# Performance work log

Measured on AMD Instinct MI355X. Metric: run time of the kernel, lower is better.

Reference implementation:

```python
import jax, jax.numpy as jnp
import numpy as np

D = 768       # input embedding dim
H = 256       # hidden_dim
NH = 4        # num_heads
HD = H // NH  # head_dim = 64
M = 131072    # number of candidate LLM embeddings


def setup_inputs() -> dict:
    key = jax.random.key(0)
    ks = jax.random.split(key, 16)
    s = 0.02
    return {
        "user": jax.random.normal(ks[0], (D,), jnp.float32),
        "query": jax.random.normal(ks[1], (D,), jnp.float32),
        "llm": jax.random.normal(ks[2], (M, D), jnp.float32),
        # projection weights (torch Linear: y = x @ W.T + b)
        "Wu": jax.random.normal(ks[3], (H, D), jnp.float32) * s,
        "bu": jnp.zeros((H,), jnp.float32),
        "Wq": jax.random.normal(ks[4], (H, D), jnp.float32) * s,
        "bq": jnp.zeros((H,), jnp.float32),
        "Wl": jax.random.normal(ks[5], (H, D), jnp.float32) * s,
        "bl": jnp.zeros((H,), jnp.float32),
        # MultiheadAttention packed in-projection [3H, H] and bias [3H]
        "in_proj_w": jax.random.normal(ks[6], (3 * H, H), jnp.float32) * s,
        "in_proj_b": jnp.zeros((3 * H,), jnp.float32),
        "out_proj_w": jax.random.normal(ks[7], (H, H), jnp.float32) * s,
        "out_proj_b": jnp.zeros((H,), jnp.float32),
        # final scoring linear: [1, 2H]
        "Wo": jax.random.normal(ks[8], (1, 2 * H), jnp.float32) * s,
        "bo": jnp.zeros((1,), jnp.float32),
    }


def reference(user, query, llm, Wu, bu, Wq, bq, Wl, bl,
              in_proj_w, in_proj_b, out_proj_w, out_proj_b, Wo, bo):
    m = llm.shape[0]
    # input projections
    u = user @ Wu.T + bu            # [H]
    qv = query @ Wq.T + bq          # [H]
    l = llm @ Wl.T + bl             # [M, H]
    # context rows are identical for every candidate -> compute K/V once on [2, H]
    ctx = jnp.stack([u, qv], axis=0)                      # [2, H]
    Wq_a, Wk_a, Wv_a = jnp.split(in_proj_w, 3, axis=0)    # each [H, H]
    bq_a, bk_a, bv_a = jnp.split(in_proj_b, 3, axis=0)
    q = (l @ Wq_a.T + bq_a).reshape(m, NH, HD)            # [M, nh, hd] (seq_len=1)
    k = (ctx @ Wk_a.T + bk_a).reshape(2, NH, HD)          # [2, nh, hd]
    v = (ctx @ Wv_a.T + bv_a).reshape(2, NH, HD)
    scale = 1.0 / jnp.sqrt(jnp.asarray(HD, q.dtype))
    scores = jnp.einsum('mhd,khd->mhk', q, k) * scale     # [M, nh, 2]
    attn = jax.nn.softmax(scores, axis=-1)
    attended = jnp.einsum('mhk,khd->mhd', attn, v).reshape(m, H)
    attended = attended @ out_proj_w.T + out_proj_b       # [M, H]
    x = jnp.concatenate([attended, l], axis=-1)           # [M, 2H]
    # out = Sequential(ReLU, Dropout(eval=identity), Linear(2H, 1))
    logits = (jax.nn.relu(x) @ Wo.T + bo).squeeze(-1)     # [M]
    return logits
```

## Files before the change

kernel.cpp:

```cpp
#include <hip/hip_runtime.h>


typedef float f32x4 __attribute__((ext_vector_type(4)));
typedef __bf16 bf16x8 __attribute__((ext_vector_type(8)));

__device__ __forceinline__ unsigned f2bf(float f) {
  unsigned u = __builtin_bit_cast(unsigned, f);
  u += 0x7fffu + ((u >> 16) & 1u);
  return u >> 16;
}

__device__ __forceinline__ void gl_lds16(const void* g, void* l) {
  __builtin_amdgcn_global_load_lds(
      (const __attribute__((address_space(1))) void*)g,
      (__attribute__((address_space(3))) void*)l, 16, 0, 0);
}

__global__ void prep_a(const float* __restrict__ user, const float* __restrict__ query,
                       const float* __restrict__ Wu, const float* __restrict__ bu,
                       const float* __restrict__ Wq, const float* __restrict__ bq,
                       float* __restrict__ wf) {
  const int og = threadIdx.x >> 5, ln = threadIdx.x & 31;
  const int o = blockIdx.x * 8 + og;
  const int isq = o >> 8, j = o & 255;
  const float* Wrow = (isq ? Wq : Wu) + (size_t)j * 768;
  const float* vec = isq ? query : user;
  float p = 0.f;
  #pragma unroll
  for (int i = 0; i < 24; ++i) { int d = ln * 24 + i; p = fmaf(Wrow[d], vec[d], p); }
  #pragma unroll
  for (int off = 16; off; off >>= 1) p += __shfl_xor(p, off);
  if (ln == 0) wf[o] = p + (isq ? bq[j] : bu[j]);
}

__global__ void prep_b(const float* __restrict__ ipw, const float* __restrict__ ipb,
                       float* __restrict__ wf) {
  const int og = threadIdx.x >> 5, ln = threadIdx.x & 31;
  const int o = blockIdx.x * 8 + og;
  const int kv = o >> 9, cc = (o >> 8) & 1, j = o & 255;
  const int row = 256 + kv * 256 + j;
  const float* Wrow = ipw + (size_t)row * 256;
  const float* ctx = wf + cc * 256;
  float p = 0.f;
  #pragma unroll
  for (int i = 0; i < 8; ++i) { int d = ln * 8 + i; p = fmaf(Wrow[d], ctx[d], p); }
  #pragma unroll
  for (int off = 16; off; off >>= 1) p += __shfl_xor(p, off);
  if (ln == 0) wf[512 + o] = p + ipb[row];
}

__global__ void prep_c(const float* __restrict__ ipw, const float* __restrict__ ipb,
                       const float* __restrict__ opw, const float* __restrict__ opb,
                       float* __restrict__ wf) {
  const int t = threadIdx.x, b = blockIdx.x;
  if (b < 4) {
    const int h = b;
    float acc = 0.f;
    for (int d = 0; d < 64; ++d) {
      float kd = wf[512 + h * 64 + d] - wf[768 + h * 64 + d];
      acc = fmaf(ipw[(size_t)(h * 64 + d) * 256 + t], kd, acc);
    }
    wf[1536 + h * 256 + t] = 0.125f * acc;
    if (t == 0) {
      float cs = 0.f;
      for (int d = 0; d < 64; ++d)
        cs = fmaf(ipb[h * 64 + d], wf[512 + h * 64 + d] - wf[768 + h * 64 + d], cs);
      wf[3840 + h] = 0.125f * cs;
    }
  } else {
    const float* oprow = opw + (size_t)t * 256;
    float bse = 0.f;
    for (int i = 0; i < 256; ++i) bse = fmaf(oprow[i], wf[1280 + i], bse);
    wf[2560 + t] = bse + opb[t];
    #pragma unroll
    for (int h = 0; h < 4; ++h) {
      float dl = 0.f;
      for (int d = 0; d < 64; ++d)
        dl = fmaf(oprow[h * 64 + d], wf[1024 + h * 64 + d] - wf[1280 + h * 64 + d], dl);
      wf[2816 + h * 256 + t] = dl;
    }
  }
}

__global__ void prep_w(const float* __restrict__ Wl, unsigned int* __restrict__ Bs4) {
  const int tid = blockIdx.x * 256 + threadIdx.x;
  const int lane = tid & 63;
  const int ntk = tid >> 6;
  const int kk = ntk >> 4, nt = ntk & 15;
  const int k = kk * 32 + (lane >> 4) * 8;
  const int j = nt * 16 + (lane & 15);
  const float* src = Wl + (size_t)j * 768 + k;
  uint4 pk;
  pk.x = f2bf(src[0]) | (f2bf(src[1]) << 16);
  pk.y = f2bf(src[2]) | (f2bf(src[3]) << 16);
  pk.z = f2bf(src[4]) | (f2bf(src[5]) << 16);
  pk.w = f2bf(src[6]) | (f2bf(src[7]) << 16);
  ((uint4*)Bs4)[tid] = pk;
}

__global__ __launch_bounds__(256, 2) void fused_main(
    const float* __restrict__ llm, const float* __restrict__ bl,
    const float* __restrict__ Wo, const float* __restrict__ bo,
    const float* __restrict__ wf, float* __restrict__ out) {

  __shared__ __align__(16) char smem[49152];
  __shared__ float csd_s[4];
  __shared__ float a_s[64][4];
  __shared__ float r2_s[64];
  __shared__ float p2_s[4][64];

  const int t = threadIdx.x;
  const int w = t >> 6, l = t & 63, g = l >> 4, c = l & 15;
  const int m0 = blockIdx.x * 64;
  const char* BsB = (const char*)(wf + 4096);

  auto stage = [&](int buf, int kk) {
    char* abase = smem + buf * 8192 + w * 1024;
    #pragma unroll
    for (int r = 0; r < 2; ++r) {
      const int chunk = r * 256 + w * 64 + l;
      const int row = chunk >> 3;
      const int cb = (chunk & 7) * 16;
      const int cl = cb ^ ((row & 7) << 4);
      const char* gp = (const char*)(llm + (size_t)(m0 + row) * 768 + kk * 32) + cl;
      gl_lds16(gp, abase + r * 4096);
    }
    char* bbase = smem + 16384 + buf * 16384 + w * 1024;
    const char* gb = BsB + (size_t)kk * 16384;
    #pragma unroll
    for (int r = 0; r < 4; ++r) {
      const int chunk = r * 256 + w * 64 + l;
      gl_lds16(gb + (size_t)chunk * 16, bbase + r * 4096);
    }
  };

  stage(0, 0);
  __syncthreads();

  f32x4 acc[16] = {};
  const int row_l = w * 16 + c;
  const int sro = row_l * 128;
  const int sxor = (row_l & 7) << 4;

  for (int kk = 0; kk < 24; ++kk) {
    const int cur = kk & 1;
    if (kk < 23) stage(cur ^ 1, kk + 1);

    const char* ab = smem + cur * 8192 + sro;
    const float4 fa = *(const float4*)(ab + ((g * 32) ^ sxor));
    const float4 fb = *(const float4*)(ab + ((g * 32 + 16) ^ sxor));
    uint4 pk;
    pk.x = f2bf(fa.x) | (f2bf(fa.y) << 16);
    pk.y = f2bf(fa.z) | (f2bf(fa.w) << 16);
    pk.z = f2bf(fb.x) | (f2bf(fb.y) << 16);
    pk.w = f2bf(fb.z) | (f2bf(fb.w) << 16);
    const bf16x8 afr = __builtin_bit_cast(bf16x8, pk);

    const char* bb = smem + 16384 + cur * 16384 + l * 16;
    #pragma unroll
    for (int nt = 0; nt < 16; ++nt) {
      const bf16x8 bfr = *(const bf16x8*)(bb + nt * 1024);
      acc[nt] = __builtin_amdgcn_mfma_f32_16x16x32_bf16(afr, bfr, acc[nt], 0, 0, 0);
    }
    __syncthreads();
  }

  float* wsd_s  = (float*)smem;
  float* delta_s = (float*)smem + 1024;
  float* base_s = (float*)smem + 2048;
  float* woa_s  = (float*)smem + 2304;
  float* wo2_s  = (float*)smem + 2560;
  float* bl_s   = (float*)smem + 2816;
  for (int i = t; i < 1024; i += 256) { wsd_s[i] = wf[1536 + i]; delta_s[i] = wf[2816 + i]; }
  base_s[t] = wf[2560 + t];
  woa_s[t] = Wo[t];
  wo2_s[t] = Wo[256 + t];
  bl_s[t] = bl[t];
  if (t < 4) csd_s[t] = wf[3840 + t];
  __syncthreads();

  float psd[4][4] = {};
  float pr2[4] = {};
  #pragma unroll
  for (int nt = 0; nt < 16; ++nt) {
    const int col = nt * 16 + c;
    const float w0 = wsd_s[col], w1 = wsd_s[256 + col], w2 = wsd_s[512 + col], w3 = wsd_s[768 + col];
    const float wo = wo2_s[col], bb2 = bl_s[col];
    #pragma unroll
    for (int j = 0; j < 4; ++j) {
      const float x = acc[nt][j] + bb2;
      psd[j][0] = fmaf(x, w0, psd[j][0]);
      psd[j][1] = fmaf(x, w1, psd[j][1]);
      psd[j][2] = fmaf(x, w2, psd[j][2]);
      psd[j][3] = fmaf(x, w3, psd[j][3]);
      pr2[j] = fmaf(fmaxf(x, 0.f), wo, pr2[j]);
    }
  }
  #pragma unroll
  for (int off = 8; off; off >>= 1) {
    #pragma unroll
    for (int j = 0; j < 4; ++j) {
      #pragma unroll
      for (int h = 0; h < 4; ++h) psd[j][h] += __shfl_xor(psd[j][h], off);
      pr2[j] += __shfl_xor(pr2[j], off);
    }
  }
  if (c == 0) {
    #pragma unroll
    for (int j = 0; j < 4; ++j) {
      const int r = w * 16 + g * 4 + j;
      #pragma unroll
      for (int h = 0; h < 4; ++h)
        a_s[r][h] = 1.f / (1.f + __expf(-(psd[j][h] + csd_s[h])));
      r2_s[r] = pr2[j];
    }
  }
  __syncthreads();

  {
    const int r = t & 63, q = t >> 6;
    const float a0 = a_s[r][0], a1 = a_s[r][1], a2 = a_s[r][2], a3 = a_s[r][3];
    float p = 0.f;
    const int j0 = q * 64;
    #pragma unroll 4
    for (int j = j0; j < j0 + 64; ++j) {
      float att = base_s[j];
      att = fmaf(a0, delta_s[j], att);
      att = fmaf(a1, delta_s[256 + j], att);
      att = fmaf(a2, delta_s[512 + j], att);
      att = fmaf(a3, delta_s[768 + j], att);
      p = fmaf(fmaxf(att, 0.f), woa_s[j], p);
    }
    p2_s[q][r] = p;
  }
  __syncthreads();
  if (t < 64)
    out[m0 + t] = p2_s[0][t] + p2_s[1][t] + p2_s[2][t] + p2_s[3][t] + r2_s[t] + bo[0];
}

extern "C" void kernel_launch(void* const* d_in, const int* in_sizes, int n_in,
                              void* d_out, int out_size, void* d_ws, size_t ws_size,
                              hipStream_t stream) {
  const float* user  = (const float*)d_in[0];
  const float* query = (const float*)d_in[1];
  const float* llm   = (const float*)d_in[2];
  const float* Wu    = (const float*)d_in[3];
  const float* bu    = (const float*)d_in[4];
  const float* Wq    = (const float*)d_in[5];
  const float* bq    = (const float*)d_in[6];
  const float* Wl    = (const float*)d_in[7];
  const float* bl    = (const float*)d_in[8];
  const float* ipw   = (const float*)d_in[9];
  const float* ipb   = (const float*)d_in[10];
  const float* opw   = (const float*)d_in[11];
  const float* opb   = (const float*)d_in[12];
  const float* Wo    = (const float*)d_in[13];
  const float* bo    = (const float*)d_in[14];
  float* out = (float*)d_out;
  float* wf = (float*)d_ws;
  unsigned int* Bs4 = (unsigned int*)(wf + 4096);

  prep_a<<<64, 256, 0, stream>>>(user, query, Wu, bu, Wq, bq, wf);
  prep_w<<<96, 256, 0, stream>>>(Wl, Bs4);
  prep_b<<<128, 256, 0, stream>>>(ipw, ipb, wf);
  prep_c<<<5, 256, 0, stream>>>(ipw, ipb, opw, opb, wf);
  fused_main<<<131072 / 64, 256, 0, stream>>>(llm, bl, Wo, bo, wf, out);
}
```

Baseline: 169.3 us.

## Triple-buffer main GEMM loads with vmcnt waits and merge prep kernels

The main kernel's k-loop moves from double to triple buffering of the LLM rows and the bf16 Wl tiles in LDS, staging two steps ahead. It replaces __syncthreads with explicit s_waitcnt vmcnt counts plus raw barriers so loads stay in flight across iterations. The four small prep kernels are merged into one launch, with the weight repack in 96 blocks and the chained context/attention precomputation serialized in a single block through shared memory. This removes launch overhead and load latency stalls, but LDS use rises to about 72KB per block, which may limit occupancy, and the single-block prep chain does serial dot products.

```diff
diff --git a/kernel.cpp b/kernel.cpp
--- a/kernel.cpp
+++ b/kernel.cpp
@@ -3,6 +3,8 @@
 
 typedef float f32x4 __attribute__((ext_vector_type(4)));
 typedef __bf16 bf16x8 __attribute__((ext_vector_type(8)));
+
+#define VMCNT(n) asm volatile("s_waitcnt vmcnt(" #n ")" ::: "memory")
 
 __device__ __forceinline__ unsigned f2bf(float f) {
   unsigned u = __builtin_bit_cast(unsigned, f);
@@ -16,86 +18,78 @@
       (__attribute__((address_space(3))) void*)l, 16, 0, 0);
 }
 
-__global__ void prep_a(const float* __restrict__ user, const float* __restrict__ query,
-                       const float* __restrict__ Wu, const float* __restrict__ bu,
-                       const float* __restrict__ Wq, const float* __restrict__ bq,
-                       float* __restrict__ wf) {
-  const int og = threadIdx.x >> 5, ln = threadIdx.x & 31;
-  const int o = blockIdx.x * 8 + og;
-  const int isq = o >> 8, j = o & 255;
-  const float* Wrow = (isq ? Wq : Wu) + (size_t)j * 768;
-  const float* vec = isq ? query : user;
-  float p = 0.f;
-  #pragma unroll
-  for (int i = 0; i < 24; ++i) { int d = ln * 24 + i; p = fmaf(Wrow[d], vec[d], p); }
-  #pragma unroll
-  for (int off = 16; off; off >>= 1) p += __shfl_xor(p, off);
-  if (ln == 0) wf[o] = p + (isq ? bq[j] : bu[j]);
-}
-
-__global__ void prep_b(const float* __restrict__ ipw, const float* __restrict__ ipb,
-                       float* __restrict__ wf) {
-  const int og = threadIdx.x >> 5, ln = threadIdx.x & 31;
-  const int o = blockIdx.x * 8 + og;
-  const int kv = o >> 9, cc = (o >> 8) & 1, j = o & 255;
-  const int row = 256 + kv * 256 + j;
-  const float* Wrow = ipw + (size_t)row * 256;
-  const float* ctx = wf + cc * 256;
-  float p = 0.f;
-  #pragma unroll
-  for (int i = 0; i < 8; ++i) { int d = ln * 8 + i; p = fmaf(Wrow[d], ctx[d], p); }
-  #pragma unroll
-  for (int off = 16; off; off >>= 1) p += __shfl_xor(p, off);
-  if (ln == 0) wf[512 + o] = p + ipb[row];
-}
-
-__global__ void prep_c(const float* __restrict__ ipw, const float* __restrict__ ipb,
-                       const float* __restrict__ opw, const float* __restrict__ opb,
-                       float* __restrict__ wf) {
-  const int t = threadIdx.x, b = blockIdx.x;
-  if (b < 4) {
-    const int h = b;
+__global__ void prep_all(const float* __restrict__ user, const float* __restrict__ query,
+                         const float* __restrict__ Wu, const float* __restrict__ bu,
+                         const float* __restrict__ Wq, const float* __restrict__ bq,
+                         const float* __restrict__ Wl,
+                         const float* __restrict__ ipw, const float* __restrict__ ipb,
+                         const float* __restrict__ opw, const float* __restrict__ opb,
+                         float* __restrict__ wf, unsigned int* __restrict__ Bs4) {
+  const int t = threadIdx.x;
+  if (blockIdx.x < 96) {
+    const int tid = blockIdx.x * 256 + t;
+    const int lane = tid & 63;
+    const int ntk = tid >> 6;
+    const int kk = ntk >> 4, nt = ntk & 15;
+    const int k = kk * 32 + (lane >> 4) * 8;
+    const int j = nt * 16 + (lane & 15);
+    const float* src = Wl + (size_t)j * 768 + k;
+    uint4 pk;
+    pk.x = f2bf(src[0]) | (f2bf(src[1]) << 16);
+    pk.y = f2bf(src[2]) | (f2bf(src[3]) << 16);
+    pk.z = f2bf(src[4]) | (f2bf(src[5]) << 16);
+    pk.w = f2bf(src[6]) | (f2bf(src[7]) << 16);
+    ((uint4*)Bs4)[tid] = pk;
+    return;
+  }
+  __shared__ float sh[1536];
+  for (int o = t; o < 512; o += 256) {
+    const int isq = o >> 8, j = o & 255;
+    const float* Wrow = (isq ? Wq : Wu) + (size_t)j * 768;
+    const float* vec = isq ? query : user;
+    float p = 0.f;
+    for (int d = 0; d < 768; ++d) p = fmaf(Wrow[d], vec[d], p);
+    p += (isq ? bq[j] : bu[j]);
+    sh[o] = p; wf[o] = p;
+  }
+  __syncthreads();
+  for (int o = t; o < 1024; o += 256) {
+    const int kv = o >> 9, cc = (o >> 8) & 1, j = o & 255;
+    const int row = 256 + kv * 256 + j;
+    const float* Wrow = ipw + (size_t)row * 256;
+    const float* ctx = sh + cc * 256;
+    float p = 0.f;
+    for (int d = 0; d < 256; ++d) p = fmaf(Wrow[d], ctx[d], p);
+    p += ipb[row];
+    sh[512 + o] = p; wf[512 + o] = p;
+  }
+  __syncthreads();
+  #pragma unroll
+  for (int h = 0; h < 4; ++h) {
     float acc = 0.f;
     for (int d = 0; d < 64; ++d) {
-      float kd = wf[512 + h * 64 + d] - wf[768 + h * 64 + d];
+      const float kd = sh[512 + h * 64 + d] - sh[768 + h * 64 + d];
       acc = fmaf(ipw[(size_t)(h * 64 + d) * 256 + t], kd, acc);
     }
     wf[1536 + h * 256 + t] = 0.125f * acc;
-    if (t == 0) {
-      float cs = 0.f;
-      for (int d = 0; d < 64; ++d)
-        cs = fmaf(ipb[h * 64 + d], wf[512 + h * 64 + d] - wf[768 + h * 64 + d], cs);
-      wf[3840 + h] = 0.125f * cs;
-    }
-  } else {
-    const float* oprow = opw + (size_t)t * 256;
-    float bse = 0.f;
-    for (int i = 0; i < 256; ++i) bse = fmaf(oprow[i], wf[1280 + i], bse);
-    wf[2560 + t] = bse + opb[t];
-    #pragma unroll
-    for (int h = 0; h < 4; ++h) {
-      float dl = 0.f;
-      for (int d = 0; d < 64; ++d)
-        dl = fmaf(oprow[h * 64 + d], wf[1024 + h * 64 + d] - wf[1280 + h * 64 + d], dl);
-      wf[2816 + h * 256 + t] = dl;
-    }
-  }
-}
-
-__global__ void prep_w(const float* __restrict__ Wl, unsigned int* __restrict__ Bs4) {
-  const int tid = blockIdx.x * 256 + threadIdx.x;
-  const int lane = tid & 63;
-  const int ntk = tid >> 6;
-  const int kk = ntk >> 4, nt = ntk & 15;
-  const int k = kk * 32 + (lane >> 4) * 8;
-  const int j = nt * 16 + (lane & 15);
-  const float* src = Wl + (size_t)j * 768 + k;
-  uint4 pk;
-  pk.x = f2bf(src[0]) | (f2bf(src[1]) << 16);
-  pk.y = f2bf(src[2]) | (f2bf(src[3]) << 16);
-  pk.z = f2bf(src[4]) | (f2bf(src[5]) << 16);
-  pk.w = f2bf(src[6]) | (f2bf(src[7]) << 16);
-  ((uint4*)Bs4)[tid] = pk;
+  }
+  if (t < 4) {
+    float cs = 0.f;
+    for (int d = 0; d < 64; ++d)
+      cs = fmaf(ipb[t * 64 + d], sh[512 + t * 64 + d] - sh[768 + t * 64 + d], cs);
+    wf[3840 + t] = 0.125f * cs;
+  }
+  const float* oprow = opw + (size_t)t * 256;
+  float bse = 0.f;
+  for (int i = 0; i < 256; ++i) bse = fmaf(oprow[i], sh[1280 + i], bse);
+  wf[2560 + t] = bse + opb[t];
+  #pragma unroll
+  for (int h = 0; h < 4; ++h) {
+    float dl = 0.f;
+    for (int d = 0; d < 64; ++d)
+      dl = fmaf(oprow[h * 64 + d], sh[1024 + h * 64 + d] - sh[1280 + h * 64 + d], dl);
+    wf[2816 + h * 256 + t] = dl;
+  }
 }
 
 __global__ __launch_bounds__(256, 2) void fused_main(
@@ -103,7 +97,7 @@
     const float* __restrict__ Wo, const float* __restrict__ bo,
     const float* __restrict__ wf, float* __restrict__ out) {
 
-  __shared__ __align__(16) char smem[49152];
+  __shared__ __align__(16) char smem[73728];
   __shared__ float csd_s[4];
   __shared__ float a_s[64][4];
   __shared__ float r2_s[64];
@@ -125,7 +119,7 @@
       const char* gp = (const char*)(llm + (size_t)(m0 + row) * 768 + kk * 32) + cl;
       gl_lds16(gp, abase + r * 4096);
     }
-    char* bbase = smem + 16384 + buf * 16384 + w * 1024;
+    char* bbase = smem + 24576 + buf * 16384 + w * 1024;
     const char* gb = BsB + (size_t)kk * 16384;
     #pragma unroll
     for (int r = 0; r < 4; ++r) {
@@ -135,16 +129,22 @@
   };
 
   stage(0, 0);
-  __syncthreads();
+  stage(1, 1);
 
   f32x4 acc[16] = {};
   const int row_l = w * 16 + c;
   const int sro = row_l * 128;
   const int sxor = (row_l & 7) << 4;
 
+  #pragma unroll 3
   for (int kk = 0; kk < 24; ++kk) {
-    const int cur = kk & 1;
-    if (kk < 23) stage(cur ^ 1, kk + 1);
+    const int cur = kk % 3;
+    if (kk < 22) stage((kk + 2) % 3, kk + 2);
+    if (kk < 22)      VMCNT(12);
+    else if (kk < 23) VMCNT(6);
+    else              VMCNT(0);
+    __builtin_amdgcn_s_barrier();
+    __builtin_amdgcn_sched_barrier(0);
 
     const char* ab = smem + cur * 8192 + sro;
     const float4 fa = *(const float4*)(ab + ((g * 32) ^ sxor));
@@ -156,13 +156,14 @@
     pk.w = f2bf(fb.z) | (f2bf(fb.w) << 16);
     const bf16x8 afr = __builtin_bit_cast(bf16x8, pk);
 
-    const char* bb = smem + 16384 + cur * 16384 + l * 16;
+    const char* bb = smem + 24576 + cur * 16384 + l * 16;
     #pragma unroll
     for (int nt = 0; nt < 16; ++nt) {
       const bf16x8 bfr = *(const bf16x8*)(bb + nt * 1024);
       acc[nt] = __builtin_amdgcn_mfma_f32_16x16x32_bf16(afr, bfr, acc[nt], 0, 0, 0);
     }
-    __syncthreads();
+    __builtin_amdgcn_sched_barrier(0);
+    __builtin_amdgcn_s_barrier();
   }
 
   float* wsd_s  = (float*)smem;
@@ -260,9 +261,7 @@
   float* wf = (float*)d_ws;
   unsigned int* Bs4 = (unsigned int*)(wf + 4096);
 
-  prep_a<<<64, 256, 0, stream>>>(user, query, Wu, bu, Wq, bq, wf);
-  prep_w<<<96, 256, 0, stream>>>(Wl, Bs4);
-  prep_b<<<128, 256, 0, stream>>>(ipw, ipb, wf);
-  prep_c<<<5, 256, 0, stream>>>(ipw, ipb, opw, opb, wf);
+  prep_all<<<97, 256, 0, stream>>>(user, query, Wu, bu, Wq, bq, Wl,
+                                   ipw, ipb, opw, opb, wf, Bs4);
   fused_main<<<131072 / 64, 256, 0, stream>>>(llm, bl, Wo, bo, wf, out);
 }
```

Measured after the change: 278.3 us. 64.4% more time.
